# Kernel optimization log

Measured on AMD Instinct MI355X. Metric: run time of the kernel, lower is better.

## Reference

```python
import jax, jax.numpy as jnp
import numpy as np

L, B, T, D = 26, 1, 512, 768
NH, NG, HD, FF = 12, 4, 64, 2048
CACHE, V, WIN = 1536, 32000, 512
S = CACHE + T
GS = NH // NG
SOFTCAP = 50.0
EPS = 1e-6
NEG = -1e9


def _rope(base, dim, positions):
    half = dim // 2
    inv = 1.0 / (base ** (np.arange(half, dtype=np.float64) / half))
    ang = positions[:, None] * inv[None, :]              # [T, half]
    ang = np.concatenate([ang, ang], axis=-1)            # [T, dim]
    cos = np.cos(ang)[None, :, None, :].astype(np.float32)
    sin = np.sin(ang)[None, :, None, :].astype(np.float32)
    return jnp.asarray(cos), jnp.asarray(sin)


def setup_inputs() -> dict:
    key = jax.random.key(0)
    ks = iter(jax.random.split(key, 32))
    w = lambda shape: jax.random.normal(next(ks), shape, dtype=jnp.float32) * 0.02
    inp = {
        'embeddings': jax.random.normal(next(ks), (B, T, D), dtype=jnp.float32),
        'kv_cache_k': jax.random.normal(next(ks), (L, B, NG, CACHE, HD), dtype=jnp.float32),
        'kv_cache_v': jax.random.normal(next(ks), (L, B, NG, HD, CACHE), dtype=jnp.float32),
        'pre_attn_w': w((L, D)), 'w_qkv': w((L, D, (NH + 2 * NG) * HD)),
        'q_norm_w': w((L, HD)), 'k_norm_w': w((L, HD)),
        'w_out': w((L, NH * HD, D)), 'post_attn_w': w((L, D)),
        'pre_ff_w': w((L, D)), 'w_gate': w((L, D, FF)), 'w_up': w((L, D, FF)),
        'w_down': w((L, FF, D)), 'post_ff_w': w((L, D)),
        'final_norm_w': w((D,)), 'w_lm': w((D, V)),
    }
    # RoPE tables for prefill positions CACHE..CACHE+T-1 (global base 1e6, local base 1e4)
    pos = np.arange(CACHE, CACHE + T, dtype=np.float64)
    inp['pos_emb_cos'], inp['pos_emb_sin'] = _rope(1.0e6, HD, pos)
    inp['pos_emb_local_cos'], inp['pos_emb_local_sin'] = _rope(1.0e4, HD, pos)
    # causal (global) and sliding-window (local) additive masks over cache+new keys
    qpos = np.arange(CACHE, CACHE + T)[:, None]          # [T,1]
    spos = np.arange(S)[None, :]                         # [1,S]
    causal = spos <= qpos
    local = causal & (spos > qpos - WIN)
    inp['mask_global'] = jnp.asarray(np.where(causal, 0.0, NEG)[None, None].astype(np.float32))
    inp['mask_local'] = jnp.asarray(np.where(local, 0.0, NEG)[None, None].astype(np.float32))
    return inp


def rms_norm(x, weight):
    xf = x.astype(jnp.float32)
    n = xf * jax.lax.rsqrt(jnp.mean(xf * xf, axis=-1, keepdims=True) + EPS)
    return (n * (1.0 + weight)).astype(x.dtype)


def apply_rope(x, cos, sin):
    half = x.shape[-1] // 2
    rot = jnp.concatenate([-x[..., half:], x[..., :half]], axis=-1)
    return x * cos + rot * sin


def reference(embeddings, mask_global, mask_local, pos_emb_cos, pos_emb_sin,
              pos_emb_local_cos, pos_emb_local_sin, kv_cache_k, kv_cache_v,
              pre_attn_w, w_qkv, q_norm_w, k_norm_w, w_out, post_attn_w,
              pre_ff_w, w_gate, w_up, w_down, post_ff_w, final_norm_w, w_lm):
    h = embeddings
    scale = 1.0 / jnp.sqrt(jnp.float32(HD))
    for i in range(L):
        is_local = (i + 1) % 6 == 0
        cos = pos_emb_local_cos if is_local else pos_emb_cos
        sin = pos_emb_local_sin if is_local else pos_emb_sin
        mask = mask_local if is_local else mask_global      # [B,1,T,S]
        x = rms_norm(h, pre_attn_w[i])
        qkv = (x @ w_qkv[i]).reshape(B, T, NG, GS + 2, HD)
        q = qkv[:, :, :, :GS, :].reshape(B, T, NH, HD)
        k = qkv[:, :, :, GS, :]                             # [B,T,NG,HD]
        v = qkv[:, :, :, GS + 1, :]                         # [B,T,NG,HD]
        q = apply_rope(rms_norm(q, q_norm_w[i]), cos, sin)
        k = apply_rope(rms_norm(k, k_norm_w[i]), cos, sin)
        k_new = jnp.transpose(k, (0, 2, 1, 3))              # [B,NG,T,HD]
        v_new = jnp.transpose(v, (0, 2, 3, 1))              # [B,NG,HD,T]
        k_full = jnp.concatenate([kv_cache_k[i], k_new], axis=2)   # [B,NG,S,HD]
        v_full = jnp.concatenate([kv_cache_v[i], v_new], axis=3)   # [B,NG,HD,S]
        # native GQA: fold heads into [NG, GS] instead of repeat_interleave on K/V
        q_g = jnp.transpose(q, (0, 2, 1, 3)).reshape(B, NG, GS, T, HD)
        scores = jnp.einsum('bgntd,bgsd->bgnts', q_g, k_full) * scale
        scores = jnp.tanh(scores / SOFTCAP) * SOFTCAP
        scores = scores + mask[:, :, None]                  # broadcast over (NG,GS)
        probs = jax.nn.softmax(scores.astype(jnp.float32), axis=-1).astype(q.dtype)
        attn = jnp.einsum('bgnts,bgds->bgntd', probs, v_full)
        attn = jnp.transpose(attn.reshape(B, NH, T, HD), (0, 2, 1, 3)).reshape(B, T, NH * HD)
        h = h + rms_norm(attn @ w_out[i], post_attn_w[i])
        xf = rms_norm(h, pre_ff_w[i])
        ff = (jax.nn.gelu(xf @ w_gate[i]) * (xf @ w_up[i])) @ w_down[i]
        h = h + rms_norm(ff, post_ff_w[i])
    logits = rms_norm(h, final_norm_w) @ w_lm
    return logits
```

## Files before the change

kernel.cpp:

```cpp
#include <hip/hip_runtime.h>
#include <math.h>

#define TT 512
#define DD 768
#define NHH 12
#define NGG 4
#define HDD 64
#define FFF 2048
#define CCH 1536
#define SEQ 2048
#define NL 26
#define VOC 32000

typedef short bh8 __attribute__((ext_vector_type(8)));
typedef float f32x4 __attribute__((ext_vector_type(4)));

__device__ __forceinline__ float fast_tanh(float x) {
    float e = __expf(2.0f * x);
    return 1.0f - 2.0f / (e + 1.0f);
}

__device__ __forceinline__ short f2bf(float f) {
    union { float f; unsigned u; } v;
    v.f = f;
    unsigned r = v.u + 0x7fffu + ((v.u >> 16) & 1u);
    return (short)(r >> 16);
}

struct __align__(8) S4 { short v[4]; };
struct __align__(16) S8 { short v[8]; };

__global__ __launch_bounds__(256) void rmsnorm_k(const float* __restrict__ in,
                                                 const float* __restrict__ w,
                                                 float* __restrict__ out) {
    int t = blockIdx.x, tid = threadIdx.x;
    const float* row = in + (size_t)t * DD;
    float x0 = row[tid], x1 = row[tid + 256], x2 = row[tid + 512];
    float s = x0 * x0 + x1 * x1 + x2 * x2;
#pragma unroll
    for (int o = 32; o > 0; o >>= 1) s += __shfl_xor(s, o);
    __shared__ float red[4];
    if ((tid & 63) == 0) red[tid >> 6] = s;
    __syncthreads();
    s = red[0] + red[1] + red[2] + red[3];
    float r = rsqrtf(s / 768.0f + 1e-6f);
    float* orow = out + (size_t)t * DD;
    orow[tid]       = x0 * r * (1.0f + w[tid]);
    orow[tid + 256] = x1 * r * (1.0f + w[tid + 256]);
    orow[tid + 512] = x2 * r * (1.0f + w[tid + 512]);
}

__global__ __launch_bounds__(256) void addnorm_k(float* __restrict__ h,
                                                 const float* __restrict__ in,
                                                 const float* __restrict__ w) {
    int t = blockIdx.x, tid = threadIdx.x;
    const float* row = in + (size_t)t * DD;
    float x0 = row[tid], x1 = row[tid + 256], x2 = row[tid + 512];
    float s = x0 * x0 + x1 * x1 + x2 * x2;
#pragma unroll
    for (int o = 32; o > 0; o >>= 1) s += __shfl_xor(s, o);
    __shared__ float red[4];
    if ((tid & 63) == 0) red[tid >> 6] = s;
    __syncthreads();
    s = red[0] + red[1] + red[2] + red[3];
    float r = rsqrtf(s / 768.0f + 1e-6f);
    float* hrow = h + (size_t)t * DD;
    hrow[tid]       += x0 * r * (1.0f + w[tid]);
    hrow[tid + 256] += x1 * r * (1.0f + w[tid + 256]);
    hrow[tid + 512] += x2 * r * (1.0f + w[tid + 512]);
}

__global__ __launch_bounds__(256) void wtrans(const float* __restrict__ w0, short* __restrict__ o0,
                                              const float* __restrict__ w1, short* __restrict__ o1,
                                              int N, int K) {
    const float* w = blockIdx.z ? w1 : w0;
    short* o = blockIdx.z ? o1 : o0;
    int n0 = blockIdx.x * 64, k0 = blockIdx.y * 64;
    __shared__ short t[64][72];
    int tid = threadIdx.x;
#pragma unroll
    for (int it = 0; it < 4; it++) {
        int kr = (tid >> 4) + it * 16, nc = (tid & 15) * 4;
        float4 v = *(const float4*)&w[(size_t)(k0 + kr) * N + n0 + nc];
        S4 p; p.v[0] = f2bf(v.x); p.v[1] = f2bf(v.y); p.v[2] = f2bf(v.z); p.v[3] = f2bf(v.w);
        *(S4*)&t[kr][nc] = p;
    }
    __syncthreads();
#pragma unroll
    for (int it = 0; it < 2; it++) {
        int nr = tid >> 2, kb2 = (tid & 3) * 16 + it * 8;
        S8 p;
#pragma unroll
        for (int j = 0; j < 8; j++) p.v[j] = t[kb2 + j][nr];
        *(S8*)&o[(size_t)(n0 + nr) * K + k0 + kb2] = p;
    }
}

__global__ __launch_bounds__(256) void cvt_kv(const float* __restrict__ kc,
                                              const float* __restrict__ vc,
                                              short* __restrict__ kb,
                                              short* __restrict__ vb) {
    int idx = blockIdx.x * 256 + threadIdx.x;
    if (idx < 98304) {
        int e = idx * 4;
        int g = e / 98304, off = e % 98304;
        float4 v = *(const float4*)&kc[(size_t)g * 98304 + off];
        S4 p; p.v[0] = f2bf(v.x); p.v[1] = f2bf(v.y); p.v[2] = f2bf(v.z); p.v[3] = f2bf(v.w);
        *(S4*)&kb[(size_t)g * (SEQ * HDD) + off] = p;
    } else {
        int e = (idx - 98304) * 4;
        int row = e / CCH, c = e % CCH;
        float4 v = *(const float4*)&vc[(size_t)row * CCH + c];
        S4 p; p.v[0] = f2bf(v.x); p.v[1] = f2bf(v.y); p.v[2] = f2bf(v.z); p.v[3] = f2bf(v.w);
        *(S4*)&vb[(size_t)row * SEQ + c] = p;
    }
}

__global__ __launch_bounds__(256) void qkv_post(const float* __restrict__ qkv,
                                                const float* __restrict__ qnw,
                                                const float* __restrict__ knw,
                                                const float* __restrict__ cosp,
                                                const float* __restrict__ sinp,
                                                short* __restrict__ q16,
                                                short* __restrict__ kb,
                                                short* __restrict__ vb) {
    int tid = threadIdx.x;
    int lane = tid & 63, wid = tid >> 6;
    int sg = blockIdx.x * 4 + wid;
    int t = sg / 20, slot = sg % 20;
    int g = slot / 5, r = slot % 5;
    float v = qkv[(size_t)t * 1280 + slot * 64 + lane];
    if (r == 4) {
        vb[((size_t)g * HDD + lane) * SEQ + CCH + t] = f2bf(v);
        return;
    }
    float s = v * v;
#pragma unroll
    for (int o = 32; o > 0; o >>= 1) s += __shfl_xor(s, o);
    float nv = v * rsqrtf(s / 64.0f + 1e-6f);
    const float* wn = (r < 3) ? qnw : knw;
    nv *= (1.0f + wn[lane]);
    float other = __shfl_xor(nv, 32);
    float rot = (lane < 32) ? -other : other;
    float ov = nv * cosp[t * 64 + lane] + rot * sinp[t * 64 + lane];
    if (r < 3)
        q16[(((size_t)(g * 3 + r)) * TT + t) * HDD + lane] = f2bf(ov);
    else
        kb[((size_t)g * SEQ + CCH + t) * HDD + lane] = f2bf(ov);
}

template <int A_BF16, int ATOMIC>
__global__ __launch_bounds__(256) void mgemm(const void* __restrict__ Av, int lda, unsigned long long aHead,
                                             const short* __restrict__ Bt, int ldb, unsigned long long bHead, int bdiv,
                                             float* __restrict__ C, int ldc, unsigned long long cHead, int cOff,
                                             int kchunk, int nsplit) {
    int h = blockIdx.z / nsplit, kz = blockIdx.z % nsplit;
    const char* Abase = (const char*)Av + (size_t)h * aHead * (A_BF16 ? 2 : 4);
    Bt += (size_t)(h / bdiv) * bHead;
    C += (size_t)h * cHead + (size_t)h * cOff;

    __shared__ short As[64][40];
    __shared__ short Bs[64][40];

    int tid = threadIdx.x;
    int srow = tid >> 2, skp = (tid & 3) * 8;
    int m0 = blockIdx.x * 64, n0 = blockIdx.y * 64;
    int kbase = kz * kchunk;
    int lane = tid & 63, wid = tid >> 6;
    int mq = (wid >> 1) * 32, nq = (wid & 1) * 32;
    int frow = lane & 15, fk = (lane >> 4) * 8;

    f32x4 acc00 = {}, acc01 = {}, acc10 = {}, acc11 = {};

    const short* Bp = Bt + (size_t)(n0 + srow) * ldb + kbase + skp;

    for (int kc = 0; kc < kchunk; kc += 32) {
        bh8 a8, b8;
        b8 = *(const bh8*)Bp;
        Bp += 32;
        if (A_BF16) {
            const short* ap = (const short*)Abase + (size_t)(m0 + srow) * lda + kbase + kc + skp;
            a8 = *(const bh8*)ap;
        } else {
            const float* ap = (const float*)Abase + (size_t)(m0 + srow) * lda + kbase + kc + skp;
            float4 x1 = *(const float4*)ap;
            float4 x2 = *(const float4*)(ap + 4);
            a8[0] = f2bf(x1.x); a8[1] = f2bf(x1.y); a8[2] = f2bf(x1.z); a8[3] = f2bf(x1.w);
            a8[4] = f2bf(x2.x); a8[5] = f2bf(x2.y); a8[6] = f2bf(x2.z); a8[7] = f2bf(x2.w);
        }
        __syncthreads();
        *(bh8*)&As[srow][skp] = a8;
        *(bh8*)&Bs[srow][skp] = b8;
        __syncthreads();
        bh8 a0 = *(const bh8*)&As[mq + frow][fk];
        bh8 a1 = *(const bh8*)&As[mq + 16 + frow][fk];
        bh8 b0 = *(const bh8*)&Bs[nq + frow][fk];
        bh8 b1 = *(const bh8*)&Bs[nq + 16 + frow][fk];
        acc00 = __builtin_amdgcn_mfma_f32_16x16x32_bf16(a0, b0, acc00, 0, 0, 0);
        acc01 = __builtin_amdgcn_mfma_f32_16x16x32_bf16(a0, b1, acc01, 0, 0, 0);
        acc10 = __builtin_amdgcn_mfma_f32_16x16x32_bf16(a1, b0, acc10, 0, 0, 0);
        acc11 = __builtin_amdgcn_mfma_f32_16x16x32_bf16(a1, b1, acc11, 0, 0, 0);
    }

    int er = (lane >> 4) * 4, ec = lane & 15;
    int grow = m0 + mq + er, gcol = n0 + nq + ec;
#pragma unroll
    for (int r = 0; r < 4; r++) {
        float v00 = acc00[r], v01 = acc01[r], v10 = acc10[r], v11 = acc11[r];
        size_t r0 = (size_t)(grow + r) * ldc, r1 = (size_t)(grow + 16 + r) * ldc;
        if (ATOMIC) {
            atomicAdd(&C[r0 + gcol], v00);
            atomicAdd(&C[r0 + gcol + 16], v01);
            atomicAdd(&C[r1 + gcol], v10);
            atomicAdd(&C[r1 + gcol + 16], v11);
        } else {
            C[r0 + gcol] = v00;
            C[r0 + gcol + 16] = v01;
            C[r1 + gcol] = v10;
            C[r1 + gcol + 16] = v11;
        }
    }
}

__global__ __launch_bounds__(256) void softcap_softmax(const float* __restrict__ sc,
                                                       const float* __restrict__ mask,
                                                       short* __restrict__ pb) {
    int t = blockIdx.x, hh = blockIdx.y, tid = threadIdx.x;
    const float* row = sc + ((size_t)hh * TT + t) * SEQ;
    const float* mrow = mask + (size_t)t * SEQ;
    float v[8];
    float mx = -1e30f;
#pragma unroll
    for (int k2 = 0; k2 < 8; k2++) {
        int s = tid + k2 * 256;
        float x = row[s] * 0.125f;
        x = 50.0f * fast_tanh(x * 0.02f);
        x += mrow[s];
        v[k2] = x;
        mx = fmaxf(mx, x);
    }
#pragma unroll
    for (int o = 32; o > 0; o >>= 1) mx = fmaxf(mx, __shfl_xor(mx, o));
    __shared__ float red[4];
    if ((tid & 63) == 0) red[tid >> 6] = mx;
    __syncthreads();
    mx = fmaxf(fmaxf(red[0], red[1]), fmaxf(red[2], red[3]));
    float sum = 0.0f;
#pragma unroll
    for (int k2 = 0; k2 < 8; k2++) {
        v[k2] = __expf(v[k2] - mx);
        sum += v[k2];
    }
#pragma unroll
    for (int o = 32; o > 0; o >>= 1) sum += __shfl_xor(sum, o);
    __syncthreads();
    if ((tid & 63) == 0) red[tid >> 6] = sum;
    __syncthreads();
    sum = red[0] + red[1] + red[2] + red[3];
    float inv = 1.0f / sum;
    short* prow = pb + ((size_t)hh * TT + t) * SEQ;
#pragma unroll
    for (int k2 = 0; k2 < 8; k2++) prow[tid + k2 * 256] = f2bf(v[k2] * inv);
}

__global__ __launch_bounds__(256) void gelu_mul_k(const float* __restrict__ g,
                                                  const float* __restrict__ u,
                                                  short* __restrict__ o) {
    size_t i = (size_t)blockIdx.x * 256 + threadIdx.x;
    float x = g[i];
    float inner = 0.7978845608028654f * (x + 0.044715f * x * x * x);
    o[i] = f2bf(0.5f * x * (1.0f + fast_tanh(inner)) * u[i]);
}

__global__ __launch_bounds__(256) void zero4_k(float4* __restrict__ p) {
    p[(size_t)blockIdx.x * 256 + threadIdx.x] = make_float4(0.f, 0.f, 0.f, 0.f);
}

#define OFF_H    0u
#define OFF_X    393216u
#define OFF_QKV  786432u
#define OFF_ATTN 1441792u
#define OFF_AO   1835008u
#define OFF_FFO  2228224u
#define OFF_GATE 2621440u
#define OFF_UP   3670016u
#define OFF_SC   4718592u
#define F32_END  17301504u
#define BO_Q16   0u
#define BO_KB    393216u
#define BO_VB    917504u
#define BO_PB    1441792u
#define BO_GACT  14024704u
#define BO_WQ    15073280u
#define BO_WO    16056320u
#define BO_WG    16646144u
#define BO_WU    18219008u
#define BO_WD    19791872u
#define BO_LMT   21364736u

extern "C" void kernel_launch(void* const* d_in, const int* in_sizes, int n_in,
                              void* d_out, int out_size, void* d_ws, size_t ws_size,
                              hipStream_t stream) {
    const float* emb          = (const float*)d_in[0];
    const float* kcache       = (const float*)d_in[1];
    const float* vcache       = (const float*)d_in[2];
    const float* pre_attn_w   = (const float*)d_in[3];
    const float* w_qkv        = (const float*)d_in[4];
    const float* q_norm_w     = (const float*)d_in[5];
    const float* k_norm_w     = (const float*)d_in[6];
    const float* w_out        = (const float*)d_in[7];
    const float* post_attn_w  = (const float*)d_in[8];
    const float* pre_ff_w     = (const float*)d_in[9];
    const float* w_gate       = (const float*)d_in[10];
    const float* w_up         = (const float*)d_in[11];
    const float* w_down       = (const float*)d_in[12];
    const float* post_ff_w    = (const float*)d_in[13];
    const float* final_norm_w = (const float*)d_in[14];
    const float* w_lm         = (const float*)d_in[15];
    const float* pe_cos       = (const float*)d_in[16];
    const float* pe_sin       = (const float*)d_in[17];
    const float* pel_cos      = (const float*)d_in[18];
    const float* pel_sin      = (const float*)d_in[19];
    const float* mask_g       = (const float*)d_in[20];
    const float* mask_l       = (const float*)d_in[21];

    float* ws   = (float*)d_ws;
    float* h    = ws + OFF_H;
    float* x    = ws + OFF_X;
    float* qkv  = ws + OFF_QKV;
    float* attn = ws + OFF_ATTN;
    float* ao   = ws + OFF_AO;
    float* ffo  = ws + OFF_FFO;
    float* gate = ws + OFF_GATE;
    float* up   = ws + OFF_UP;
    float* sc   = ws + OFF_SC;
    short* bws  = (short*)(ws + F32_END);
    short* q16  = bws + BO_Q16;
    short* kb   = bws + BO_KB;
    short* vb   = bws + BO_VB;
    short* pb   = bws + BO_PB;
    short* gact = bws + BO_GACT;
    short* wqT  = bws + BO_WQ;
    short* woT  = bws + BO_WO;
    short* wgT  = bws + BO_WG;
    short* wuT  = bws + BO_WU;
    short* wdT  = bws + BO_WD;
    short* lmT  = bws + BO_LMT;
    float* out  = (float*)d_out;

    hipMemcpyAsync(h, emb, (size_t)TT * DD * sizeof(float), hipMemcpyDeviceToDevice, stream);

    for (int i = 0; i < NL; i++) {
        bool is_local = ((i + 1) % 6 == 0);
        const float* cosp  = is_local ? pel_cos : pe_cos;
        const float* sinp  = is_local ? pel_sin : pe_sin;
        const float* maskp = is_local ? mask_l : mask_g;
        const float* wqkv_i  = w_qkv  + (size_t)i * DD * 1280;
        const float* wout_i  = w_out  + (size_t)i * DD * DD;
        const float* wgate_i = w_gate + (size_t)i * DD * FFF;
        const float* wup_i   = w_up   + (size_t)i * DD * FFF;
        const float* wdown_i = w_down + (size_t)i * FFF * DD;
        const float* kc_i = kcache + (size_t)i * NGG * CCH * HDD;
        const float* vc_i = vcache + (size_t)i * NGG * HDD * CCH;

        zero4_k<<<1152, 256, 0, stream>>>((float4*)(ws + OFF_ATTN));

        rmsnorm_k<<<TT, 256, 0, stream>>>(h, pre_attn_w + (size_t)i * DD, x);

        wtrans<<<dim3(20, 12, 1), 256, 0, stream>>>(wqkv_i, wqT, wqkv_i, wqT, 1280, DD);

        mgemm<0, 0><<<dim3(8, 20, 1), 256, 0, stream>>>(x, DD, 0ull, wqT, DD, 0ull, 1,
                                                        qkv, 1280, 0ull, 0, 768, 1);

        cvt_kv<<<768, 256, 0, stream>>>(kc_i, vc_i, kb, vb);

        qkv_post<<<2560, 256, 0, stream>>>(qkv, q_norm_w + (size_t)i * HDD,
                                           k_norm_w + (size_t)i * HDD, cosp, sinp,
                                           q16, kb, vb);

        wtrans<<<dim3(12, 12, 1), 256, 0, stream>>>(wout_i, woT, wout_i, woT, DD, DD);

        mgemm<1, 0><<<dim3(8, 32, 12), 256, 0, stream>>>(
            q16, HDD, (unsigned long long)(TT * HDD), kb, HDD,
            (unsigned long long)(SEQ * HDD), 3, sc, SEQ,
            (unsigned long long)(TT * SEQ), 0, 64, 1);

        softcap_softmax<<<dim3(TT, NHH), 256, 0, stream>>>(sc, maskp, pb);

        mgemm<1, 1><<<dim3(8, 1, NHH * 4), 256, 0, stream>>>(
            pb, SEQ, (unsigned long long)(TT * SEQ), vb, SEQ,
            (unsigned long long)(HDD * SEQ), 3, attn, DD, 0ull, 64, 512, 4);

        mgemm<0, 1><<<dim3(8, 12, 2), 256, 0, stream>>>(attn, DD, 0ull, woT, DD, 0ull, 1,
                                                        ao, DD, 0ull, 0, 384, 2);

        addnorm_k<<<TT, 256, 0, stream>>>(h, ao, post_attn_w + (size_t)i * DD);

        rmsnorm_k<<<TT, 256, 0, stream>>>(h, pre_ff_w + (size_t)i * DD, x);
        wtrans<<<dim3(32, 12, 2), 256, 0, stream>>>(wgate_i, wgT, wup_i, wuT, FFF, DD);
        mgemm<0, 0><<<dim3(8, 32, 1), 256, 0, stream>>>(x, DD, 0ull, wgT, DD, 0ull, 1,
                                                        gate, FFF, 0ull, 0, 768, 1);
        mgemm<0, 0><<<dim3(8, 32, 1), 256, 0, stream>>>(x, DD, 0ull, wuT, DD, 0ull, 1,
                                                        up, FFF, 0ull, 0, 768, 1);
        gelu_mul_k<<<4096, 256, 0, stream>>>(gate, up, gact);
        wtrans<<<dim3(12, 32, 1), 256, 0, stream>>>(wdown_i, wdT, wdown_i, wdT, DD, FFF);
        mgemm<1, 1><<<dim3(8, 12, 4), 256, 0, stream>>>(gact, FFF, 0ull, wdT, FFF, 0ull, 1,
                                                        ffo, DD, 0ull, 0, 512, 4);
        addnorm_k<<<TT, 256, 0, stream>>>(h, ffo, post_ff_w + (size_t)i * DD);
    }

    rmsnorm_k<<<TT, 256, 0, stream>>>(h, final_norm_w, x);
    wtrans<<<dim3(500, 12, 1), 256, 0, stream>>>(w_lm, lmT, w_lm, lmT, VOC, DD);
    mgemm<0, 0><<<dim3(8, 500, 1), 256, 0, stream>>>(x, DD, 0ull, lmT, DD, 0ull, 1,
                                                     out, VOC, 0ull, 0, 768, 1);
}
```

Before: 4.528 ms.

## Double-buffer GEMM tiles via direct global-to-LDS loads, use bf16 activations, fuse gate/up

The GEMM kernel now loads 64-wide K tiles straight from global memory into XOR-swizzled shared memory using global_load_lds, with two buffers so the next tile's load overlaps the current tile's MFMAs. To allow this, every A operand must be bf16: rmsnorm writes bf16 output and a new conversion kernel turns the attention output into bf16 before the output projection. The separate gate and up GEMMs become one wider GEMM, assuming the gate and up transposed weights sit next to each other so they form 4096 columns, and gelu_mul reads both halves from one buffer. The risks are the layout assumption for the combined weights and reusing the score buffer to hold the bf16 attention copy.

```diff
diff --git a/kernel.cpp b/kernel.cpp
--- a/kernel.cpp
+++ b/kernel.cpp
@@ -30,9 +30,17 @@
 struct __align__(8) S4 { short v[4]; };
 struct __align__(16) S8 { short v[8]; };
 
+__device__ __forceinline__ void gll16(const short* g, short* l) {
+    __builtin_amdgcn_global_load_lds(
+        (const __attribute__((address_space(1))) void*)g,
+        (__attribute__((address_space(3))) void*)l, 16, 0, 0);
+}
+
+#define FIDX(r, b) ((r) * 64 + ((((b) ^ ((r) & 7))) * 8))
+
 __global__ __launch_bounds__(256) void rmsnorm_k(const float* __restrict__ in,
                                                  const float* __restrict__ w,
-                                                 float* __restrict__ out) {
+                                                 short* __restrict__ out) {
     int t = blockIdx.x, tid = threadIdx.x;
     const float* row = in + (size_t)t * DD;
     float x0 = row[tid], x1 = row[tid + 256], x2 = row[tid + 512];
@@ -44,10 +52,10 @@
     __syncthreads();
     s = red[0] + red[1] + red[2] + red[3];
     float r = rsqrtf(s / 768.0f + 1e-6f);
-    float* orow = out + (size_t)t * DD;
-    orow[tid]       = x0 * r * (1.0f + w[tid]);
-    orow[tid + 256] = x1 * r * (1.0f + w[tid + 256]);
-    orow[tid + 512] = x2 * r * (1.0f + w[tid + 512]);
+    short* orow = out + (size_t)t * DD;
+    orow[tid]       = f2bf(x0 * r * (1.0f + w[tid]));
+    orow[tid + 256] = f2bf(x1 * r * (1.0f + w[tid + 256]));
+    orow[tid + 512] = f2bf(x2 * r * (1.0f + w[tid + 512]));
 }
 
 __global__ __launch_bounds__(256) void addnorm_k(float* __restrict__ h,
@@ -149,57 +157,82 @@
         kb[((size_t)g * SEQ + CCH + t) * HDD + lane] = f2bf(ov);
 }
 
-template <int A_BF16, int ATOMIC>
-__global__ __launch_bounds__(256) void mgemm(const void* __restrict__ Av, int lda, unsigned long long aHead,
+template <int ATOMIC>
+__global__ __launch_bounds__(256) void mgemm(const short* __restrict__ A, int lda, unsigned long long aHead,
                                              const short* __restrict__ Bt, int ldb, unsigned long long bHead, int bdiv,
                                              float* __restrict__ C, int ldc, unsigned long long cHead, int cOff,
                                              int kchunk, int nsplit) {
     int h = blockIdx.z / nsplit, kz = blockIdx.z % nsplit;
-    const char* Abase = (const char*)Av + (size_t)h * aHead * (A_BF16 ? 2 : 4);
+    A  += (size_t)h * aHead;
     Bt += (size_t)(h / bdiv) * bHead;
-    C += (size_t)h * cHead + (size_t)h * cOff;
-
-    __shared__ short As[64][40];
-    __shared__ short Bs[64][40];
+    C  += (size_t)h * cHead + (size_t)h * cOff;
+
+    __shared__ short As[2][4096];
+    __shared__ short Bs[2][4096];
 
     int tid = threadIdx.x;
-    int srow = tid >> 2, skp = (tid & 3) * 8;
     int m0 = blockIdx.x * 64, n0 = blockIdx.y * 64;
     int kbase = kz * kchunk;
     int lane = tid & 63, wid = tid >> 6;
     int mq = (wid >> 1) * 32, nq = (wid & 1) * 32;
-    int frow = lane & 15, fk = (lane >> 4) * 8;
+    int frow = lane & 15;
+    int blk = lane >> 4;
+
+    int srow = tid >> 3, sblk = tid & 7;
+    int sswz = sblk ^ (srow & 7);
+    const short* Ap0 = A + (size_t)(m0 + srow) * lda + kbase + sswz * 8;
+    const short* Ap1 = A + (size_t)(m0 + srow + 32) * lda + kbase + sswz * 8;
+    const short* Bp0 = Bt + (size_t)(n0 + srow) * ldb + kbase + sswz * 8;
+    const short* Bp1 = Bt + (size_t)(n0 + srow + 32) * ldb + kbase + sswz * 8;
+    int l0 = tid * 8, l1 = 2048 + tid * 8;
+
+    int oA0a = FIDX(mq + frow, blk),      oA0b = FIDX(mq + frow, blk + 4);
+    int oA1a = FIDX(mq + 16 + frow, blk), oA1b = FIDX(mq + 16 + frow, blk + 4);
+    int oB0a = FIDX(nq + frow, blk),      oB0b = FIDX(nq + frow, blk + 4);
+    int oB1a = FIDX(nq + 16 + frow, blk), oB1b = FIDX(nq + 16 + frow, blk + 4);
 
     f32x4 acc00 = {}, acc01 = {}, acc10 = {}, acc11 = {};
 
-    const short* Bp = Bt + (size_t)(n0 + srow) * ldb + kbase + skp;
-
-    for (int kc = 0; kc < kchunk; kc += 32) {
-        bh8 a8, b8;
-        b8 = *(const bh8*)Bp;
-        Bp += 32;
-        if (A_BF16) {
-            const short* ap = (const short*)Abase + (size_t)(m0 + srow) * lda + kbase + kc + skp;
-            a8 = *(const bh8*)ap;
-        } else {
-            const float* ap = (const float*)Abase + (size_t)(m0 + srow) * lda + kbase + kc + skp;
-            float4 x1 = *(const float4*)ap;
-            float4 x2 = *(const float4*)(ap + 4);
-            a8[0] = f2bf(x1.x); a8[1] = f2bf(x1.y); a8[2] = f2bf(x1.z); a8[3] = f2bf(x1.w);
-            a8[4] = f2bf(x2.x); a8[5] = f2bf(x2.y); a8[6] = f2bf(x2.z); a8[7] = f2bf(x2.w);
+    int nt = kchunk / 64;
+
+    gll16(Ap0, &As[0][l0]);
+    gll16(Ap1, &As[0][l1]);
+    gll16(Bp0, &Bs[0][l0]);
+    gll16(Bp1, &Bs[0][l1]);
+    asm volatile("s_waitcnt vmcnt(0)" ::: "memory");
+    __syncthreads();
+
+    for (int t = 0; t < nt; t++) {
+        int cur = t & 1;
+        if (t + 1 < nt) {
+            int ko = (t + 1) * 64;
+            gll16(Ap0 + ko, &As[cur ^ 1][l0]);
+            gll16(Ap1 + ko, &As[cur ^ 1][l1]);
+            gll16(Bp0 + ko, &Bs[cur ^ 1][l0]);
+            gll16(Bp1 + ko, &Bs[cur ^ 1][l1]);
         }
-        __syncthreads();
-        *(bh8*)&As[srow][skp] = a8;
-        *(bh8*)&Bs[srow][skp] = b8;
-        __syncthreads();
-        bh8 a0 = *(const bh8*)&As[mq + frow][fk];
-        bh8 a1 = *(const bh8*)&As[mq + 16 + frow][fk];
-        bh8 b0 = *(const bh8*)&Bs[nq + frow][fk];
-        bh8 b1 = *(const bh8*)&Bs[nq + 16 + frow][fk];
-        acc00 = __builtin_amdgcn_mfma_f32_16x16x32_bf16(a0, b0, acc00, 0, 0, 0);
-        acc01 = __builtin_amdgcn_mfma_f32_16x16x32_bf16(a0, b1, acc01, 0, 0, 0);
-        acc10 = __builtin_amdgcn_mfma_f32_16x16x32_bf16(a1, b0, acc10, 0, 0, 0);
-        acc11 = __builtin_amdgcn_mfma_f32_16x16x32_bf16(a1, b1, acc11, 0, 0, 0);
+        const short* as = As[cur];
+        const short* bs = Bs[cur];
+        bh8 a0a = *(const bh8*)&as[oA0a];
+        bh8 a0b = *(const bh8*)&as[oA0b];
+        bh8 a1a = *(const bh8*)&as[oA1a];
+        bh8 a1b = *(const bh8*)&as[oA1b];
+        bh8 b0a = *(const bh8*)&bs[oB0a];
+        bh8 b0b = *(const bh8*)&bs[oB0b];
+        bh8 b1a = *(const bh8*)&bs[oB1a];
+        bh8 b1b = *(const bh8*)&bs[oB1b];
+        acc00 = __builtin_amdgcn_mfma_f32_16x16x32_bf16(a0a, b0a, acc00, 0, 0, 0);
+        acc00 = __builtin_amdgcn_mfma_f32_16x16x32_bf16(a0b, b0b, acc00, 0, 0, 0);
+        acc01 = __builtin_amdgcn_mfma_f32_16x16x32_bf16(a0a, b1a, acc01, 0, 0, 0);
+        acc01 = __builtin_amdgcn_mfma_f32_16x16x32_bf16(a0b, b1b, acc01, 0, 0, 0);
+        acc10 = __builtin_amdgcn_mfma_f32_16x16x32_bf16(a1a, b0a, acc10, 0, 0, 0);
+        acc10 = __builtin_amdgcn_mfma_f32_16x16x32_bf16(a1b, b0b, acc10, 0, 0, 0);
+        acc11 = __builtin_amdgcn_mfma_f32_16x16x32_bf16(a1a, b1a, acc11, 0, 0, 0);
+        acc11 = __builtin_amdgcn_mfma_f32_16x16x32_bf16(a1b, b1b, acc11, 0, 0, 0);
+        if (t + 1 < nt) {
+            asm volatile("s_waitcnt vmcnt(0)" ::: "memory");
+            __syncthreads();
+        }
     }
 
     int er = (lane >> 4) * 4, ec = lane & 15;
@@ -263,13 +296,22 @@
     for (int k2 = 0; k2 < 8; k2++) prow[tid + k2 * 256] = f2bf(v[k2] * inv);
 }
 
-__global__ __launch_bounds__(256) void gelu_mul_k(const float* __restrict__ g,
-                                                  const float* __restrict__ u,
+__global__ __launch_bounds__(256) void gelu_mul_k(const float* __restrict__ gu,
                                                   short* __restrict__ o) {
     size_t i = (size_t)blockIdx.x * 256 + threadIdx.x;
-    float x = g[i];
+    int t = (int)(i >> 11), f = (int)(i & 2047);
+    float x = gu[(size_t)t * 4096 + f];
+    float u = gu[(size_t)t * 4096 + 2048 + f];
     float inner = 0.7978845608028654f * (x + 0.044715f * x * x * x);
-    o[i] = f2bf(0.5f * x * (1.0f + fast_tanh(inner)) * u[i]);
+    o[i] = f2bf(0.5f * x * (1.0f + fast_tanh(inner)) * u);
+}
+
+__global__ __launch_bounds__(256) void cvt_bf16_k(const float* __restrict__ in,
+                                                  short* __restrict__ out) {
+    int i = blockIdx.x * 256 + threadIdx.x;
+    float4 v = ((const float4*)in)[i];
+    S4 p; p.v[0] = f2bf(v.x); p.v[1] = f2bf(v.y); p.v[2] = f2bf(v.z); p.v[3] = f2bf(v.w);
+    ((S4*)out)[i] = p;
 }
 
 __global__ __launch_bounds__(256) void zero4_k(float4* __restrict__ p) {
@@ -326,14 +368,14 @@
 
     float* ws   = (float*)d_ws;
     float* h    = ws + OFF_H;
-    float* x    = ws + OFF_X;
+    short* xb   = (short*)(ws + OFF_X);
     float* qkv  = ws + OFF_QKV;
     float* attn = ws + OFF_ATTN;
     float* ao   = ws + OFF_AO;
     float* ffo  = ws + OFF_FFO;
     float* gate = ws + OFF_GATE;
-    float* up   = ws + OFF_UP;
     float* sc   = ws + OFF_SC;
+    short* attnb= (short*)(ws + OFF_SC);
     short* bws  = (short*)(ws + F32_END);
     short* q16  = bws + BO_Q16;
     short* kb   = bws + BO_KB;
@@ -365,12 +407,12 @@
 
         zero4_k<<<1152, 256, 0, stream>>>((float4*)(ws + OFF_ATTN));
 
-        rmsnorm_k<<<TT, 256, 0, stream>>>(h, pre_attn_w + (size_t)i * DD, x);
+        rmsnorm_k<<<TT, 256, 0, stream>>>(h, pre_attn_w + (size_t)i * DD, xb);
 
         wtrans<<<dim3(20, 12, 1), 256, 0, stream>>>(wqkv_i, wqT, wqkv_i, wqT, 1280, DD);
 
-        mgemm<0, 0><<<dim3(8, 20, 1), 256, 0, stream>>>(x, DD, 0ull, wqT, DD, 0ull, 1,
-                                                        qkv, 1280, 0ull, 0, 768, 1);
+        mgemm<0><<<dim3(8, 20, 1), 256, 0, stream>>>(xb, DD, 0ull, wqT, DD, 0ull, 1,
+                                                     qkv, 1280, 0ull, 0, 768, 1);
 
         cvt_kv<<<768, 256, 0, stream>>>(kc_i, vc_i, kb, vb);
 
@@ -380,37 +422,37 @@
 
         wtrans<<<dim3(12, 12, 1), 256, 0, stream>>>(wout_i, woT, wout_i, woT, DD, DD);
 
-        mgemm<1, 0><<<dim3(8, 32, 12), 256, 0, stream>>>(
+        mgemm<0><<<dim3(8, 32, 12), 256, 0, stream>>>(
             q16, HDD, (unsigned long long)(TT * HDD), kb, HDD,
             (unsigned long long)(SEQ * HDD), 3, sc, SEQ,
             (unsigned long long)(TT * SEQ), 0, 64, 1);
 
         softcap_softmax<<<dim3(TT, NHH), 256, 0, stream>>>(sc, maskp, pb);
 
-        mgemm<1, 1><<<dim3(8, 1, NHH * 4), 256, 0, stream>>>(
+        mgemm<1><<<dim3(8, 1, NHH * 4), 256, 0, stream>>>(
             pb, SEQ, (unsigned long long)(TT * SEQ), vb, SEQ,
             (unsigned long long)(HDD * SEQ), 3, attn, DD, 0ull, 64, 512, 4);
 
-        mgemm<0, 1><<<dim3(8, 12, 2), 256, 0, stream>>>(attn, DD, 0ull, woT, DD, 0ull, 1,
-                                                        ao, DD, 0ull, 0, 384, 2);
+        cvt_bf16_k<<<384, 256, 0, stream>>>(attn, attnb);
+
+        mgemm<1><<<dim3(8, 12, 2), 256, 0, stream>>>(attnb, DD, 0ull, woT, DD, 0ull, 1,
+                                                     ao, DD, 0ull, 0, 384, 2);
 
         addnorm_k<<<TT, 256, 0, stream>>>(h, ao, post_attn_w + (size_t)i * DD);
 
-        rmsnorm_k<<<TT, 256, 0, stream>>>(h, pre_ff_w + (size_t)i * DD, x);
+        rmsnorm_k<<<TT, 256, 0, stream>>>(h, pre_ff_w + (size_t)i * DD, xb);
         wtrans<<<dim3(32, 12, 2), 256, 0, stream>>>(wgate_i, wgT, wup_i, wuT, FFF, DD);
-        mgemm<0, 0><<<dim3(8, 32, 1), 256, 0, stream>>>(x, DD, 0ull, wgT, DD, 0ull, 1,
-                                                        gate, FFF, 0ull, 0, 768, 1);
-        mgemm<0, 0><<<dim3(8, 32, 1), 256, 0, stream>>>(x, DD, 0ull, wuT, DD, 0ull, 1,
-                                                        up, FFF, 0ull, 0, 768, 1);
-        gelu_mul_k<<<4096, 256, 0, stream>>>(gate, up, gact);
+        mgemm<0><<<dim3(8, 64, 1), 256, 0, stream>>>(xb, DD, 0ull, wgT, DD, 0ull, 1,
+                                                     gate, 4096, 0ull, 0, 768, 1);
+        gelu_mul_k<<<4096, 256, 0, stream>>>(gate, gact);
         wtrans<<<dim3(12, 32, 1), 256, 0, stream>>>(wdown_i, wdT, wdown_i, wdT, DD, FFF);
-        mgemm<1, 1><<<dim3(8, 12, 4), 256, 0, stream>>>(gact, FFF, 0ull, wdT, FFF, 0ull, 1,
-                                                        ffo, DD, 0ull, 0, 512, 4);
+        mgemm<1><<<dim3(8, 12, 4), 256, 0, stream>>>(gact, FFF, 0ull, wdT, FFF, 0ull, 1,
+                                                     ffo, DD, 0ull, 0, 512, 4);
         addnorm_k<<<TT, 256, 0, stream>>>(h, ffo, post_ff_w + (size_t)i * DD);
     }
 
-    rmsnorm_k<<<TT, 256, 0, stream>>>(h, final_norm_w, x);
+    rmsnorm_k<<<TT, 256, 0, stream>>>(h, final_norm_w, xb);
     wtrans<<<dim3(500, 12, 1), 256, 0, stream>>>(w_lm, lmT, w_lm, lmT, VOC, DD);
-    mgemm<0, 0><<<dim3(8, 500, 1), 256, 0, stream>>>(x, DD, 0ull, lmT, DD, 0ull, 1,
-                                                     out, VOC, 0ull, 0, 768, 1);
-}
+    mgemm<0><<<dim3(8, 500, 1), 256, 0, stream>>>(xb, DD, 0ull, lmT, DD, 0ull, 1,
+                                                  out, VOC, 0ull, 0, 768, 1);
+}
```

New measurement: 3.683 ms. 1.23x faster.
